# Kernel tuning notes

Hardware: AMD Instinct MI355X
Metric: run time of the kernel (lower is better)

Reference implementation:

```python
import jax, jax.numpy as jnp
import numpy as np

B, S, D = 2, 2048, 1024
N_HEADS = 16
HEAD_DIM = D // N_HEADS


def setup_inputs() -> dict:
    key = jax.random.key(0)
    k1, k2, k3, k4, k5 = jax.random.split(key, 5)
    query = jax.random.normal(k1, (B, S, D), dtype=jnp.float32)
    key_t = jax.random.normal(k2, (B, S, D), dtype=jnp.float32)
    value = jax.random.normal(k3, (B, S, D), dtype=jnp.float32)
    # nn.Linear(dim, 3*dim): weight [3D, D], bias [3D]
    lim = 1.0 / np.sqrt(D)
    W_qkv_w = jax.random.uniform(k4, (3 * D, D), dtype=jnp.float32, minval=-lim, maxval=lim)
    W_qkv_b = jax.random.uniform(k5, (3 * D,), dtype=jnp.float32, minval=-lim, maxval=lim)
    return {"query": query, "key": key_t, "value": value, "W_qkv_w": W_qkv_w, "W_qkv_b": W_qkv_b}


def reference(query, key, value, W_qkv_w, W_qkv_b):
    # key/value args are ignored by the original module: Q, K, V all come
    # from the fused projection of `query` (faithful to source).
    b, s, d = query.shape
    qkv = query @ W_qkv_w.T + W_qkv_b                      # [B, S, 3D]
    qkv = qkv.reshape(b, s, 3, N_HEADS, HEAD_DIM)
    qkv = jnp.transpose(qkv, (2, 0, 3, 1, 4))              # [3, B, H, S, dh]
    q, k, v = qkv[0], qkv[1], qkv[2]
    # Faithful (inverted) scaling: scores DIVIDED by sqrt(1/d_model)
    scale_factor = jnp.sqrt(jnp.asarray(1.0 / (HEAD_DIM * N_HEADS), dtype=query.dtype))
    scores = jnp.einsum('bhqd,bhkd->bhqk', q, k) / scale_factor
    attn = jax.nn.softmax(scores, axis=-1)                 # dropout p=0.0 -> identity
    out = jnp.einsum('bhqk,bhkd->bhqd', attn, v)           # [B, H, S, dh]
    out = jnp.transpose(out, (0, 2, 1, 3)).reshape(b, s, d)
    return out
```

## Files before the change

### kernel.cpp

```cpp
#include <hip/hip_runtime.h>

#define B_  2
#define S_  2048
#define D_  1024
#define H_  16
#define DH_ 64
#define BH_ (B_*H_)
#define NT_ (S_/64)

using f32x4   = __attribute__((ext_vector_type(4))) float;
using short4v = __attribute__((ext_vector_type(4))) short;
using short8v = __attribute__((ext_vector_type(8))) short;

__device__ short g_qh[(size_t)BH_*S_*DH_];
__device__ short g_ql[(size_t)BH_*S_*DH_];
__device__ short g_kh[(size_t)BH_*S_*DH_];
__device__ short g_kl[(size_t)BH_*S_*DH_];
__device__ short g_vt[(size_t)BH_*DH_*S_];

__device__ __forceinline__ short f2bf(float x){
  unsigned u = __builtin_bit_cast(unsigned, x);
  u += 0x7fffu + ((u >> 16) & 1u);
  return (short)(unsigned short)(u >> 16);
}
__device__ __forceinline__ float bf2f(short h){
  return __builtin_bit_cast(float, ((unsigned)(unsigned short)h) << 16);
}
__device__ __forceinline__ void split4f(const float4 v, short4v& h4, short4v& l4){
  float f[4] = {v.x, v.y, v.z, v.w};
#pragma unroll
  for (int i = 0; i < 4; ++i){
    short hh = f2bf(f[i]);
    h4[i] = hh;
    l4[i] = f2bf(f[i] - bf2f(hh));
  }
}

#define MFMA16(A,B,C) __builtin_amdgcn_mfma_f32_16x16x32_bf16((A),(B),(C),0,0,0)

__global__ __launch_bounds__(256) void qkv_proj_mfma(
    const float* __restrict__ X, const float* __restrict__ W,
    const float* __restrict__ bias)
{
  __shared__ short SM[20480];
  short (*AH )[40] = (short(*)[40])(SM);
  short (*AL )[40] = (short(*)[40])(SM + 5120);
  short (*BHs)[40] = (short(*)[40])(SM + 10240);
  short (*BLs)[40] = (short(*)[40])(SM + 15360);
  short *LT = SM;

  const int tid = threadIdx.x;
  const int w  = tid >> 6;
  const int ln = tid & 15;
  const int g  = (tid & 63) >> 4;
  const int wr = w >> 1, wc = w & 1;
  const int m0 = blockIdx.y * 128;
  const int n0 = blockIdx.x * 128;
  const int which = n0 >> 10;

  f32x4 zero4 = {0.f, 0.f, 0.f, 0.f};
  f32x4 acc[4][4];
#pragma unroll
  for (int mf = 0; mf < 4; ++mf)
#pragma unroll
    for (int nf = 0; nf < 4; ++nf) acc[mf][nf] = zero4;

  float4 xa[4], wb[4];
#pragma unroll
  for (int rep = 0; rep < 4; ++rep) {
    int idx = rep * 256 + tid;
    int r  = idx >> 3;
    int c4 = (idx & 7) << 2;
    xa[rep] = *(const float4*)&X[(size_t)(m0 + r) * D_ + c4];
    wb[rep] = *(const float4*)&W[(size_t)(n0 + r) * D_ + c4];
  }

  for (int k0 = 0; k0 < D_; k0 += 32) {
#pragma unroll
    for (int rep = 0; rep < 4; ++rep) {
      int idx = rep * 256 + tid;
      int r  = idx >> 3;
      int c4 = (idx & 7) << 2;
      short4v ah4, al4, bh4, bl4;
      split4f(xa[rep], ah4, al4);
      split4f(wb[rep], bh4, bl4);
      *(short4v*)&AH [r][c4] = ah4;
      *(short4v*)&BHs[r][c4] = bh4;
      if (which < 2) {
        *(short4v*)&AL [r][c4] = al4;
        *(short4v*)&BLs[r][c4] = bl4;
      }
    }
    __syncthreads();

    if (k0 + 32 < D_) {
#pragma unroll
      for (int rep = 0; rep < 4; ++rep) {
        int idx = rep * 256 + tid;
        int r  = idx >> 3;
        int c4 = (idx & 7) << 2;
        xa[rep] = *(const float4*)&X[(size_t)(m0 + r) * D_ + k0 + 32 + c4];
        wb[rep] = *(const float4*)&W[(size_t)(n0 + r) * D_ + k0 + 32 + c4];
      }
    }

    short8v ah[4], al[4], bhf[4], blf[4];
#pragma unroll
    for (int mf = 0; mf < 4; ++mf) {
      ah[mf] = *(const short8v*)&AH[64*wr + 16*mf + ln][8*g];
      if (which < 2) al[mf] = *(const short8v*)&AL[64*wr + 16*mf + ln][8*g];
    }
#pragma unroll
    for (int nf = 0; nf < 4; ++nf) {
      bhf[nf] = *(const short8v*)&BHs[64*wc + 16*nf + ln][8*g];
      if (which < 2) blf[nf] = *(const short8v*)&BLs[64*wc + 16*nf + ln][8*g];
    }
#pragma unroll
    for (int mf = 0; mf < 4; ++mf)
#pragma unroll
      for (int nf = 0; nf < 4; ++nf) {
        acc[mf][nf] = MFMA16(ah[mf], bhf[nf], acc[mf][nf]);
        if (which < 2) {
          acc[mf][nf] = MFMA16(al[mf], bhf[nf], acc[mf][nf]);
          acc[mf][nf] = MFMA16(ah[mf], blf[nf], acc[mf][nf]);
        }
      }
    __syncthreads();
  }

  const float sc = (which == 0) ? 32.0f : 1.0f;
  float bb[4];
#pragma unroll
  for (int nf = 0; nf < 4; ++nf) bb[nf] = bias[n0 + 64*wc + 16*nf + ln];
#pragma unroll
  for (int mf = 0; mf < 4; ++mf)
#pragma unroll
    for (int nf = 0; nf < 4; ++nf)
#pragma unroll
      for (int i = 0; i < 4; ++i)
        acc[mf][nf][i] = (acc[mf][nf][i] + bb[nf]) * sc;

  const int bidx  = m0 >> 11;
  const int s0    = m0 & 2047;
  const int hbase = (n0 & 1023) >> 6;

  if (which == 2) {
#pragma unroll
    for (int nf = 0; nf < 4; ++nf) {
      int dl = 64*wc + 16*nf + ln;
#pragma unroll
      for (int mf = 0; mf < 4; ++mf) {
        int sl = 64*wr + 16*mf + 4*g;
        short4v v4;
#pragma unroll
        for (int i = 0; i < 4; ++i) v4[i] = f2bf(acc[mf][nf][i]);
        *(short4v*)&LT[dl*136 + sl] = v4;
      }
    }
    __syncthreads();
#pragma unroll
    for (int rep = 0; rep < 8; ++rep) {
      int idx = rep * 256 + tid;
      int r  = idx >> 4;
      int sg = idx & 15;
      short8v v = *(const short8v*)&LT[r*136 + sg*8];
      int h = hbase + (r >> 6), dh = r & 63;
      *(short8v*)&g_vt[(((size_t)(bidx*H_ + h))*DH_ + dh)*S_ + s0 + sg*8] = v;
    }
  } else {
    short* dH = (which == 0) ? g_qh : g_kh;
    short* dL = (which == 0) ? g_ql : g_kl;
#pragma unroll
    for (int mf = 0; mf < 4; ++mf)
#pragma unroll
      for (int nf = 0; nf < 4; ++nf) {
        int dl = 64*wc + 16*nf + ln;
#pragma unroll
        for (int i = 0; i < 4; ++i)
          LT[(64*wr + 16*mf + 4*g + i)*136 + dl] = f2bf(acc[mf][nf][i]);
      }
    __syncthreads();
#pragma unroll
    for (int rep = 0; rep < 8; ++rep) {
      int idx = rep * 256 + tid;
      int r  = idx >> 4;
      int sg = idx & 15;
      short8v v = *(const short8v*)&LT[r*136 + sg*8];
      int h = hbase + (sg >> 3);
      int dh = (sg & 7) * 8;
      *(short8v*)&dH[(((size_t)(bidx*H_ + h))*S_ + s0 + r)*DH_ + dh] = v;
    }
    __syncthreads();
#pragma unroll
    for (int mf = 0; mf < 4; ++mf)
#pragma unroll
      for (int nf = 0; nf < 4; ++nf) {
        int dl = 64*wc + 16*nf + ln;
#pragma unroll
        for (int i = 0; i < 4; ++i) {
          float v = acc[mf][nf][i];
          short hi = f2bf(v);
          LT[(64*wr + 16*mf + 4*g + i)*136 + dl] = f2bf(v - bf2f(hi));
        }
      }
    __syncthreads();
#pragma unroll
    for (int rep = 0; rep < 8; ++rep) {
      int idx = rep * 256 + tid;
      int r  = idx >> 4;
      int sg = idx & 15;
      short8v v = *(const short8v*)&LT[r*136 + sg*8];
      int h = hbase + (sg >> 3);
      int dh = (sg & 7) * 8;
      *(short8v*)&dL[(((size_t)(bidx*H_ + h))*S_ + s0 + r)*DH_ + dh] = v;
    }
  }
}

__global__ __launch_bounds__(256, 2) void attn_mfma(float* __restrict__ out)
{
  __shared__ short PS[4][32][64];

  const int tid = threadIdx.x;
  const int w  = tid >> 6;
  const int ln = tid & 15;
  const int g  = (tid & 63) >> 4;

  const int bid = blockIdx.x;
  const int swz = (bid & 7) * 64 + (bid >> 3);
  const int bh  = swz >> 4;
  const int q0  = (swz & 15) * 128;
  const int b   = bh >> 4, h = bh & 15;

  const size_t qb = (size_t)bh * S_ * DH_;
  const short* __restrict__ Kh = g_kh + qb;
  const short* __restrict__ Kl = g_kl + qb;
  const short* __restrict__ Vt = g_vt + (size_t)bh * DH_ * S_;

  short8v qh[2][2], ql[2][2];
#pragma unroll
  for (int rf = 0; rf < 2; ++rf)
#pragma unroll
    for (int ks = 0; ks < 2; ++ks) {
      size_t o = qb + (size_t)(q0 + 32*w + 16*rf + ln) * DH_ + 32*ks + 8*g;
      qh[rf][ks] = *(const short8v*)&g_qh[o];
      ql[rf][ks] = *(const short8v*)&g_ql[o];
    }

  f32x4 zero4 = {0.f,0.f,0.f,0.f};
  f32x4 o_[2][4];
  float m_[2][4], l_[2][4];
#pragma unroll
  for (int rf = 0; rf < 2; ++rf)
#pragma unroll
    for (int nf = 0; nf < 4; ++nf) o_[rf][nf] = zero4;
#pragma unroll
  for (int rf = 0; rf < 2; ++rf)
#pragma unroll
    for (int i = 0; i < 4; ++i) { m_[rf][i] = -1e30f; l_[rf][i] = 0.f; }

  for (int t = 0; t < NT_; ++t) {
    const int t0 = t * 64;

    short8v kh[2][4], kl[2][4];
#pragma unroll
    for (int ks = 0; ks < 2; ++ks)
#pragma unroll
      for (int nf = 0; nf < 4; ++nf) {
        size_t o = (size_t)(t0 + 16*nf + ln) * DH_ + 32*ks + 8*g;
        kh[ks][nf] = *(const short8v*)&Kh[o];
        kl[ks][nf] = *(const short8v*)&Kl[o];
      }

    f32x4 s[2][4];
#pragma unroll
    for (int rf = 0; rf < 2; ++rf)
#pragma unroll
      for (int nf = 0; nf < 4; ++nf) s[rf][nf] = zero4;
#pragma unroll
    for (int rf = 0; rf < 2; ++rf)
#pragma unroll
      for (int ks = 0; ks < 2; ++ks)
#pragma unroll
        for (int nf = 0; nf < 4; ++nf) {
          s[rf][nf] = MFMA16(qh[rf][ks], kh[ks][nf], s[rf][nf]);
          s[rf][nf] = MFMA16(ql[rf][ks], kh[ks][nf], s[rf][nf]);
          s[rf][nf] = MFMA16(qh[rf][ks], kl[ks][nf], s[rf][nf]);
        }

    short8v vb[2][4];
#pragma unroll
    for (int ks = 0; ks < 2; ++ks)
#pragma unroll
      for (int nf = 0; nf < 4; ++nf)
        vb[ks][nf] = *(const short8v*)&Vt[(size_t)(16*nf + ln) * S_ + t0 + 32*ks + 8*g];

#pragma unroll
    for (int rf = 0; rf < 2; ++rf)
#pragma unroll
      for (int i = 0; i < 4; ++i) {
        float mt = fmaxf(fmaxf(s[rf][0][i], s[rf][1][i]),
                         fmaxf(s[rf][2][i], s[rf][3][i]));
        mt = fmaxf(mt, __shfl_xor(mt, 1));
        mt = fmaxf(mt, __shfl_xor(mt, 2));
        mt = fmaxf(mt, __shfl_xor(mt, 4));
        mt = fmaxf(mt, __shfl_xor(mt, 8));
        float mn = fmaxf(m_[rf][i], mt);
        float corr = __expf(m_[rf][i] - mn);
        float sum = 0.f;
#pragma unroll
        for (int nf = 0; nf < 4; ++nf) {
          float p = __expf(s[rf][nf][i] - mn);
          sum += p;
          s[rf][nf][i] = p;
        }
        sum += __shfl_xor(sum, 1);
        sum += __shfl_xor(sum, 2);
        sum += __shfl_xor(sum, 4);
        sum += __shfl_xor(sum, 8);
        l_[rf][i] = l_[rf][i] * corr + sum;
        m_[rf][i] = mn;
        const int row = 16*rf + 4*g + i;
        const int e   = (4*g + i) & 7;
#pragma unroll
        for (int nf = 0; nf < 4; ++nf) {
          o_[rf][nf][i] *= corr;
          PS[w][row][(16*nf + ln) ^ (e << 3)] = f2bf(s[rf][nf][i]);
        }
      }

#pragma unroll
    for (int rf = 0; rf < 2; ++rf)
#pragma unroll
      for (int ks = 0; ks < 2; ++ks) {
        const short8v pa =
            *(const short8v*)&PS[w][16*rf + ln][(32*ks + 8*g) ^ ((ln & 7) << 3)];
#pragma unroll
        for (int nf = 0; nf < 4; ++nf)
          o_[rf][nf] = MFMA16(pa, vb[ks][nf], o_[rf][nf]);
      }
  }

#pragma unroll
  for (int rf = 0; rf < 2; ++rf)
#pragma unroll
    for (int i = 0; i < 4; ++i) {
      float inv = 1.0f / l_[rf][i];
      int row = q0 + 32*w + 16*rf + 4*g + i;
      float* op = &out[((size_t)b * S_ + row) * D_ + h * DH_];
#pragma unroll
      for (int nf = 0; nf < 4; ++nf)
        op[16*nf + ln] = o_[rf][nf][i] * inv;
    }
}

extern "C" void kernel_launch(void* const* d_in, const int* in_sizes, int n_in,
                              void* d_out, int out_size, void* d_ws, size_t ws_size,
                              hipStream_t stream) {
    (void)d_ws; (void)ws_size; (void)n_in; (void)in_sizes;
    const float* X    = (const float*)d_in[0];
    const float* W    = (const float*)d_in[3];
    const float* bias = (const float*)d_in[4];
    float* out = (float*)d_out;

    dim3 gProj(24, 32);
    qkv_proj_mfma<<<gProj, 256, 0, stream>>>(X, W, bias);

    attn_mfma<<<dim3(512), 256, 0, stream>>>(out);
}
```

Before: 318.3 us.

## Pre-split inputs to bf16 hi/lo, shrink attention tiles, use exp2 and lazy rescale

Adds a separate pass that splits X and W into bf16 hi/lo arrays once, so the projection GEMM loads ready-made bf16 instead of converting fp32 inside every tile. The attention kernel now gives each block 64 query rows (16 per wave), doubling the grid and targeting four blocks per CU. The Q scale folds in log2(e) so softmax can use exp2f, and the running-max correction is skipped when no row's max grew. s_setprio hints are placed around the MFMA sections. The split pass costs extra global memory traffic and two more launches, and each K/V tile is now reloaded by twice as many blocks.

```diff
diff --git a/kernel.cpp b/kernel.cpp
--- a/kernel.cpp
+++ b/kernel.cpp
@@ -7,11 +7,14 @@
 #define DH_ 64
 #define BH_ (B_*H_)
 #define NT_ (S_/64)
+#define QSCALE 46.1662413084f
 
 using f32x4   = __attribute__((ext_vector_type(4))) float;
 using short4v = __attribute__((ext_vector_type(4))) short;
 using short8v = __attribute__((ext_vector_type(8))) short;
 
+__device__ short g_xh[(size_t)B_*S_*D_], g_xl[(size_t)B_*S_*D_];
+__device__ short g_wh[(size_t)3*D_*D_],  g_wl[(size_t)3*D_*D_];
 __device__ short g_qh[(size_t)BH_*S_*DH_];
 __device__ short g_ql[(size_t)BH_*S_*DH_];
 __device__ short g_kh[(size_t)BH_*S_*DH_];
@@ -26,21 +29,32 @@
 __device__ __forceinline__ float bf2f(short h){
   return __builtin_bit_cast(float, ((unsigned)(unsigned short)h) << 16);
 }
-__device__ __forceinline__ void split4f(const float4 v, short4v& h4, short4v& l4){
-  float f[4] = {v.x, v.y, v.z, v.w};
-#pragma unroll
-  for (int i = 0; i < 4; ++i){
-    short hh = f2bf(f[i]);
-    h4[i] = hh;
-    l4[i] = f2bf(f[i] - bf2f(hh));
-  }
-}
 
 #define MFMA16(A,B,C) __builtin_amdgcn_mfma_f32_16x16x32_bf16((A),(B),(C),0,0,0)
 
-__global__ __launch_bounds__(256) void qkv_proj_mfma(
-    const float* __restrict__ X, const float* __restrict__ W,
-    const float* __restrict__ bias)
+__global__ __launch_bounds__(256) void split_f32(
+    const float* __restrict__ src, short* __restrict__ dh,
+    short* __restrict__ dl, int n8)
+{
+  int i = blockIdx.x * 256 + threadIdx.x;
+  const int stride = gridDim.x * 256;
+  for (; i < n8; i += stride) {
+    float4 a = ((const float4*)src)[2*i];
+    float4 b = ((const float4*)src)[2*i + 1];
+    float f[8] = {a.x,a.y,a.z,a.w,b.x,b.y,b.z,b.w};
+    short8v h, l;
+#pragma unroll
+    for (int j = 0; j < 8; ++j) {
+      short hh = f2bf(f[j]);
+      h[j] = hh;
+      l[j] = f2bf(f[j] - bf2f(hh));
+    }
+    ((short8v*)dh)[i] = h;
+    ((short8v*)dl)[i] = l;
+  }
+}
+
+__global__ __launch_bounds__(256) void qkv_proj_mfma(const float* __restrict__ bias)
 {
   __shared__ short SM[20480];
   short (*AH )[40] = (short(*)[40])(SM);
@@ -58,6 +72,9 @@
   const int n0 = blockIdx.x * 128;
   const int which = n0 >> 10;
 
+  const int r_  = tid >> 2;
+  const int c8  = (tid & 3) << 3;
+
   f32x4 zero4 = {0.f, 0.f, 0.f, 0.f};
   f32x4 acc[4][4];
 #pragma unroll
@@ -65,42 +82,43 @@
 #pragma unroll
     for (int nf = 0; nf < 4; ++nf) acc[mf][nf] = zero4;
 
-  float4 xa[4], wb[4];
-#pragma unroll
-  for (int rep = 0; rep < 4; ++rep) {
-    int idx = rep * 256 + tid;
-    int r  = idx >> 3;
-    int c4 = (idx & 7) << 2;
-    xa[rep] = *(const float4*)&X[(size_t)(m0 + r) * D_ + c4];
-    wb[rep] = *(const float4*)&W[(size_t)(n0 + r) * D_ + c4];
+  short8v rAh[2], rAl[2], rBh[2], rBl[2];
+#pragma unroll
+  for (int rep = 0; rep < 2; ++rep) {
+    size_t ao = (size_t)(m0 + 64*rep + r_) * D_ + c8;
+    size_t bo = (size_t)(n0 + 64*rep + r_) * D_ + c8;
+    rAh[rep] = *(const short8v*)&g_xh[ao];
+    rBh[rep] = *(const short8v*)&g_wh[bo];
+    if (which < 2) {
+      rAl[rep] = *(const short8v*)&g_xl[ao];
+      rBl[rep] = *(const short8v*)&g_wl[bo];
+    }
   }
 
   for (int k0 = 0; k0 < D_; k0 += 32) {
 #pragma unroll
-    for (int rep = 0; rep < 4; ++rep) {
-      int idx = rep * 256 + tid;
-      int r  = idx >> 3;
-      int c4 = (idx & 7) << 2;
-      short4v ah4, al4, bh4, bl4;
-      split4f(xa[rep], ah4, al4);
-      split4f(wb[rep], bh4, bl4);
-      *(short4v*)&AH [r][c4] = ah4;
-      *(short4v*)&BHs[r][c4] = bh4;
+    for (int rep = 0; rep < 2; ++rep) {
+      int r = 64*rep + r_;
+      *(short8v*)&AH [r][c8] = rAh[rep];
+      *(short8v*)&BHs[r][c8] = rBh[rep];
       if (which < 2) {
-        *(short4v*)&AL [r][c4] = al4;
-        *(short4v*)&BLs[r][c4] = bl4;
+        *(short8v*)&AL [r][c8] = rAl[rep];
+        *(short8v*)&BLs[r][c8] = rBl[rep];
       }
     }
     __syncthreads();
 
     if (k0 + 32 < D_) {
 #pragma unroll
-      for (int rep = 0; rep < 4; ++rep) {
-        int idx = rep * 256 + tid;
-        int r  = idx >> 3;
-        int c4 = (idx & 7) << 2;
-        xa[rep] = *(const float4*)&X[(size_t)(m0 + r) * D_ + k0 + 32 + c4];
-        wb[rep] = *(const float4*)&W[(size_t)(n0 + r) * D_ + k0 + 32 + c4];
+      for (int rep = 0; rep < 2; ++rep) {
+        size_t ao = (size_t)(m0 + 64*rep + r_) * D_ + k0 + 32 + c8;
+        size_t bo = (size_t)(n0 + 64*rep + r_) * D_ + k0 + 32 + c8;
+        rAh[rep] = *(const short8v*)&g_xh[ao];
+        rBh[rep] = *(const short8v*)&g_wh[bo];
+        if (which < 2) {
+          rAl[rep] = *(const short8v*)&g_xl[ao];
+          rBl[rep] = *(const short8v*)&g_wl[bo];
+        }
       }
     }
 
@@ -115,6 +133,7 @@
       bhf[nf] = *(const short8v*)&BHs[64*wc + 16*nf + ln][8*g];
       if (which < 2) blf[nf] = *(const short8v*)&BLs[64*wc + 16*nf + ln][8*g];
     }
+    __builtin_amdgcn_s_setprio(1);
 #pragma unroll
     for (int mf = 0; mf < 4; ++mf)
 #pragma unroll
@@ -125,10 +144,11 @@
           acc[mf][nf] = MFMA16(ah[mf], blf[nf], acc[mf][nf]);
         }
       }
-    __syncthreads();
-  }
-
-  const float sc = (which == 0) ? 32.0f : 1.0f;
+    __builtin_amdgcn_s_setprio(0);
+    __syncthreads();
+  }
+
+  const float sc = (which == 0) ? QSCALE : 1.0f;
   float bb[4];
 #pragma unroll
   for (int nf = 0; nf < 4; ++nf) bb[nf] = bias[n0 + 64*wc + 16*nf + ln];
@@ -217,9 +237,9 @@
   }
 }
 
-__global__ __launch_bounds__(256, 2) void attn_mfma(float* __restrict__ out)
+__global__ __launch_bounds__(256, 4) void attn_mfma(float* __restrict__ out)
 {
-  __shared__ short PS[4][32][64];
+  __shared__ short PS[4][16][64];
 
   const int tid = threadIdx.x;
   const int w  = tid >> 6;
@@ -227,9 +247,9 @@
   const int g  = (tid & 63) >> 4;
 
   const int bid = blockIdx.x;
-  const int swz = (bid & 7) * 64 + (bid >> 3);
-  const int bh  = swz >> 4;
-  const int q0  = (swz & 15) * 128;
+  const int swz = (bid & 7) * 128 + (bid >> 3);
+  const int bh  = swz >> 5;
+  const int q0  = (swz & 31) * 64;
   const int b   = bh >> 4, h = bh & 15;
 
   const size_t qb = (size_t)bh * S_ * DH_;
@@ -237,27 +257,21 @@
   const short* __restrict__ Kl = g_kl + qb;
   const short* __restrict__ Vt = g_vt + (size_t)bh * DH_ * S_;
 
-  short8v qh[2][2], ql[2][2];
-#pragma unroll
-  for (int rf = 0; rf < 2; ++rf)
-#pragma unroll
-    for (int ks = 0; ks < 2; ++ks) {
-      size_t o = qb + (size_t)(q0 + 32*w + 16*rf + ln) * DH_ + 32*ks + 8*g;
-      qh[rf][ks] = *(const short8v*)&g_qh[o];
-      ql[rf][ks] = *(const short8v*)&g_ql[o];
-    }
+  short8v qh[2], ql[2];
+#pragma unroll
+  for (int ks = 0; ks < 2; ++ks) {
+    size_t o = qb + (size_t)(q0 + 16*w + ln) * DH_ + 32*ks + 8*g;
+    qh[ks] = *(const short8v*)&g_qh[o];
+    ql[ks] = *(const short8v*)&g_ql[o];
+  }
 
   f32x4 zero4 = {0.f,0.f,0.f,0.f};
-  f32x4 o_[2][4];
-  float m_[2][4], l_[2][4];
-#pragma unroll
-  for (int rf = 0; rf < 2; ++rf)
-#pragma unroll
-    for (int nf = 0; nf < 4; ++nf) o_[rf][nf] = zero4;
-#pragma unroll
-  for (int rf = 0; rf < 2; ++rf)
-#pragma unroll
-    for (int i = 0; i < 4; ++i) { m_[rf][i] = -1e30f; l_[rf][i] = 0.f; }
+  f32x4 o_[4];
+  float m_[4], l_[4];
+#pragma unroll
+  for (int nf = 0; nf < 4; ++nf) o_[nf] = zero4;
+#pragma unroll
+  for (int i = 0; i < 4; ++i) { m_[i] = -1e30f; l_[i] = 0.f; }
 
   for (int t = 0; t < NT_; ++t) {
     const int t0 = t * 64;
@@ -272,21 +286,19 @@
         kl[ks][nf] = *(const short8v*)&Kl[o];
       }
 
-    f32x4 s[2][4];
-#pragma unroll
-    for (int rf = 0; rf < 2; ++rf)
-#pragma unroll
-      for (int nf = 0; nf < 4; ++nf) s[rf][nf] = zero4;
-#pragma unroll
-    for (int rf = 0; rf < 2; ++rf)
-#pragma unroll
-      for (int ks = 0; ks < 2; ++ks)
-#pragma unroll
-        for (int nf = 0; nf < 4; ++nf) {
-          s[rf][nf] = MFMA16(qh[rf][ks], kh[ks][nf], s[rf][nf]);
-          s[rf][nf] = MFMA16(ql[rf][ks], kh[ks][nf], s[rf][nf]);
-          s[rf][nf] = MFMA16(qh[rf][ks], kl[ks][nf], s[rf][nf]);
-        }
+    f32x4 s[4];
+#pragma unroll
+    for (int nf = 0; nf < 4; ++nf) s[nf] = zero4;
+    __builtin_amdgcn_s_setprio(1);
+#pragma unroll
+    for (int ks = 0; ks < 2; ++ks)
+#pragma unroll
+      for (int nf = 0; nf < 4; ++nf) {
+        s[nf] = MFMA16(qh[ks], kh[ks][nf], s[nf]);
+        s[nf] = MFMA16(ql[ks], kh[ks][nf], s[nf]);
+        s[nf] = MFMA16(qh[ks], kl[ks][nf], s[nf]);
+      }
+    __builtin_amdgcn_s_setprio(0);
 
     short8v vb[2][4];
 #pragma unroll
@@ -295,63 +307,68 @@
       for (int nf = 0; nf < 4; ++nf)
         vb[ks][nf] = *(const short8v*)&Vt[(size_t)(16*nf + ln) * S_ + t0 + 32*ks + 8*g];
 
-#pragma unroll
-    for (int rf = 0; rf < 2; ++rf)
+    float mt[4];
+#pragma unroll
+    for (int i = 0; i < 4; ++i) {
+      float v = fmaxf(fmaxf(s[0][i], s[1][i]), fmaxf(s[2][i], s[3][i]));
+      v = fmaxf(v, __shfl_xor(v, 1));
+      v = fmaxf(v, __shfl_xor(v, 2));
+      v = fmaxf(v, __shfl_xor(v, 4));
+      v = fmaxf(v, __shfl_xor(v, 8));
+      mt[i] = v;
+    }
+    bool need = (mt[0] > m_[0]) | (mt[1] > m_[1]) |
+                (mt[2] > m_[2]) | (mt[3] > m_[3]);
+    if (__any(need)) {
 #pragma unroll
       for (int i = 0; i < 4; ++i) {
-        float mt = fmaxf(fmaxf(s[rf][0][i], s[rf][1][i]),
-                         fmaxf(s[rf][2][i], s[rf][3][i]));
-        mt = fmaxf(mt, __shfl_xor(mt, 1));
-        mt = fmaxf(mt, __shfl_xor(mt, 2));
-        mt = fmaxf(mt, __shfl_xor(mt, 4));
-        mt = fmaxf(mt, __shfl_xor(mt, 8));
-        float mn = fmaxf(m_[rf][i], mt);
-        float corr = __expf(m_[rf][i] - mn);
-        float sum = 0.f;
-#pragma unroll
-        for (int nf = 0; nf < 4; ++nf) {
-          float p = __expf(s[rf][nf][i] - mn);
-          sum += p;
-          s[rf][nf][i] = p;
-        }
-        sum += __shfl_xor(sum, 1);
-        sum += __shfl_xor(sum, 2);
-        sum += __shfl_xor(sum, 4);
-        sum += __shfl_xor(sum, 8);
-        l_[rf][i] = l_[rf][i] * corr + sum;
-        m_[rf][i] = mn;
-        const int row = 16*rf + 4*g + i;
-        const int e   = (4*g + i) & 7;
-#pragma unroll
-        for (int nf = 0; nf < 4; ++nf) {
-          o_[rf][nf][i] *= corr;
-          PS[w][row][(16*nf + ln) ^ (e << 3)] = f2bf(s[rf][nf][i]);
-        }
-      }
-
-#pragma unroll
-    for (int rf = 0; rf < 2; ++rf)
-#pragma unroll
-      for (int ks = 0; ks < 2; ++ks) {
-        const short8v pa =
-            *(const short8v*)&PS[w][16*rf + ln][(32*ks + 8*g) ^ ((ln & 7) << 3)];
-#pragma unroll
-        for (int nf = 0; nf < 4; ++nf)
-          o_[rf][nf] = MFMA16(pa, vb[ks][nf], o_[rf][nf]);
-      }
-  }
-
-#pragma unroll
-  for (int rf = 0; rf < 2; ++rf)
+        float mn = fmaxf(m_[i], mt[i]);
+        float corr = exp2f(m_[i] - mn);
+        l_[i] *= corr;
+        m_[i] = mn;
+#pragma unroll
+        for (int nf = 0; nf < 4; ++nf) o_[nf][i] *= corr;
+      }
+    }
 #pragma unroll
     for (int i = 0; i < 4; ++i) {
-      float inv = 1.0f / l_[rf][i];
-      int row = q0 + 32*w + 16*rf + 4*g + i;
-      float* op = &out[((size_t)b * S_ + row) * D_ + h * DH_];
+      float sum = 0.f;
+      const int row = 4*g + i;
+      const int e   = row & 7;
+#pragma unroll
+      for (int nf = 0; nf < 4; ++nf) {
+        float p = exp2f(s[nf][i] - m_[i]);
+        sum += p;
+        PS[w][row][(16*nf + ln) ^ (e << 3)] = f2bf(p);
+      }
+      sum += __shfl_xor(sum, 1);
+      sum += __shfl_xor(sum, 2);
+      sum += __shfl_xor(sum, 4);
+      sum += __shfl_xor(sum, 8);
+      l_[i] += sum;
+    }
+
+    __builtin_amdgcn_s_setprio(1);
+#pragma unroll
+    for (int ks = 0; ks < 2; ++ks) {
+      const short8v pa =
+          *(const short8v*)&PS[w][ln][(32*ks + 8*g) ^ ((ln & 7) << 3)];
 #pragma unroll
       for (int nf = 0; nf < 4; ++nf)
-        op[16*nf + ln] = o_[rf][nf][i] * inv;
-    }
+        o_[nf] = MFMA16(pa, vb[ks][nf], o_[nf]);
+    }
+    __builtin_amdgcn_s_setprio(0);
+  }
+
+#pragma unroll
+  for (int i = 0; i < 4; ++i) {
+    float inv = 1.0f / l_[i];
+    int row = q0 + 16*w + 4*g + i;
+    float* op = &out[((size_t)b * S_ + row) * D_ + h * DH_];
+#pragma unroll
+    for (int nf = 0; nf < 4; ++nf)
+      op[16*nf + ln] = o_[nf][i] * inv;
+  }
 }
 
 extern "C" void kernel_launch(void* const* d_in, const int* in_sizes, int n_in,
@@ -363,8 +380,17 @@
     const float* bias = (const float*)d_in[4];
     float* out = (float*)d_out;
 
+    short *xh, *xl, *wh, *wl;
+    hipGetSymbolAddress((void**)&xh, HIP_SYMBOL(g_xh));
+    hipGetSymbolAddress((void**)&xl, HIP_SYMBOL(g_xl));
+    hipGetSymbolAddress((void**)&wh, HIP_SYMBOL(g_wh));
+    hipGetSymbolAddress((void**)&wl, HIP_SYMBOL(g_wl));
+
+    split_f32<<<dim3(1024), 256, 0, stream>>>(X, xh, xl, (B_*S_*D_)/8);
+    split_f32<<<dim3(1024), 256, 0, stream>>>(W, wh, wl, (3*D_*D_)/8);
+
     dim3 gProj(24, 32);
-    qkv_proj_mfma<<<gProj, 256, 0, stream>>>(X, W, bias);
-
-    attn_mfma<<<dim3(512), 256, 0, stream>>>(out);
-}
+    qkv_proj_mfma<<<gProj, 256, 0, stream>>>(bias);
+
+    attn_mfma<<<dim3(1024), 256, 0, stream>>>(out);
+}
```

Result: slower. 613.0 us (+92.6%).
